# Optimization experiments

Measured on AMD Instinct MI355X. Metric: run time of the kernel, lower is better.

## Reference

```python
import jax, jax.numpy as jnp
import numpy as np

D_MODEL = 1024
N_HEADS = 16
N_KV_HEADS = 4
HEAD_DIM = 64


def setup_inputs() -> dict:
    key = jax.random.key(0)
    ks = jax.random.split(key, 5)
    B, T, P = 2, 512, 8
    scale = 1.0 / np.sqrt(D_MODEL)
    return {
        "hidden_states": jax.random.normal(ks[0], (B, T, P, D_MODEL), dtype=jnp.float32),
        # weights stored [in, out] so y = x @ W (same math as nn.Linear with W^T)
        "Wq": jax.random.normal(ks[1], (D_MODEL, N_HEADS * HEAD_DIM), dtype=jnp.float32) * scale,
        "Wk": jax.random.normal(ks[2], (D_MODEL, N_KV_HEADS * HEAD_DIM), dtype=jnp.float32) * scale,
        "Wv": jax.random.normal(ks[3], (D_MODEL, N_KV_HEADS * HEAD_DIM), dtype=jnp.float32) * scale,
        "Wo": jax.random.normal(ks[4], (N_HEADS * HEAD_DIM, D_MODEL), dtype=jnp.float32) * scale,
    }


def _rope_tables(T, d):
    half = d // 2
    inv_freq = 1.0 / (10000.0 ** (jnp.arange(half, dtype=jnp.float32) / half))
    pos = jnp.arange(T, dtype=jnp.float32)
    angles = pos[:, None] * inv_freq[None, :]  # (T, half)
    return jnp.cos(angles), jnp.sin(angles)


def _apply_rope(x, cos, sin):
    # x: (B, P, T, H, d); cos/sin: (T, d/2)
    half = x.shape[-1] // 2
    x1, x2 = x[..., :half], x[..., half:]
    c = cos[None, None, :, None, :]
    s = sin[None, None, :, None, :]
    return jnp.concatenate([x1 * c - x2 * s, x1 * s + x2 * c], axis=-1)


def reference(hidden_states, Wq, Wk, Wv, Wo):
    B, T, P, _ = hidden_states.shape
    x = jnp.transpose(hidden_states, (0, 2, 1, 3))  # (B, P, T, C)
    q = (x @ Wq).reshape(B, P, T, N_HEADS, HEAD_DIM)
    k = (x @ Wk).reshape(B, P, T, N_KV_HEADS, HEAD_DIM)
    v = (x @ Wv).reshape(B, P, T, N_KV_HEADS, HEAD_DIM)

    rep = N_HEADS // N_KV_HEADS
    k = jnp.repeat(k, rep, axis=3)  # (B,P,T,H,d) interleaved like torch repeat/view
    v = jnp.repeat(v, rep, axis=3)

    cos, sin = _rope_tables(T, HEAD_DIM)
    q = _apply_rope(q, cos, sin)
    k = _apply_rope(k, cos, sin)

    # (B,P,H,T,d)
    q = jnp.transpose(q, (0, 1, 3, 2, 4))
    k = jnp.transpose(k, (0, 1, 3, 2, 4))
    v = jnp.transpose(v, (0, 1, 3, 2, 4))

    attn = jnp.einsum("bphqd,bphkd->bphqk", q, k) / jnp.sqrt(
        jnp.asarray(HEAD_DIM, q.dtype))
    attn = jax.nn.softmax(attn, axis=-1)
    out = jnp.einsum("bphqk,bphkd->bphqd", attn, v)
    out = jnp.transpose(out, (0, 1, 3, 2, 4)).reshape(B, P, T, N_HEADS * HEAD_DIM)
    out = jnp.transpose(out, (0, 2, 1, 3))  # (B, T, P, H*d)
    return out @ Wo
```

## Files before the change

### kernel.cpp

```cpp
#include <hip/hip_runtime.h>
#include <hip/hip_bf16.h>
#include <stdint.h>


typedef __attribute__((ext_vector_type(8))) short bf16x8;
typedef __attribute__((ext_vector_type(4))) float f32x4;
typedef __attribute__((ext_vector_type(16))) float f32x16;
typedef __attribute__((ext_vector_type(4))) unsigned short us4;
typedef __attribute__((ext_vector_type(8))) unsigned short us8;

static __device__ __forceinline__ unsigned short f2bf(float f) {
  unsigned u = __float_as_uint(f);
  u += 0x7fffu + ((u >> 16) & 1u);
  return (unsigned short)(u >> 16);
}

static __device__ __forceinline__ us8 pack8(float4 a, float4 b) {
  union { __hip_bfloat162 h[4]; us8 v; } u;
  u.h[0] = __float22bfloat162_rn(make_float2(a.x, a.y));
  u.h[1] = __float22bfloat162_rn(make_float2(a.z, a.w));
  u.h[2] = __float22bfloat162_rn(make_float2(b.x, b.y));
  u.h[3] = __float22bfloat162_rn(make_float2(b.z, b.w));
  return u.v;
}

static __device__ __forceinline__ void ld_lds16(const void* g, void* l) {
  __builtin_amdgcn_global_load_lds(
      (const __attribute__((address_space(1))) void*)g,
      (__attribute__((address_space(3))) void*)l, 16, 0, 0);
}

static __device__ __forceinline__ f32x4 mfma16(bf16x8 a, bf16x8 b, f32x4 c) {
  return __builtin_amdgcn_mfma_f32_16x16x32_bf16(a, b, c, 0, 0, 0);
}
static __device__ __forceinline__ f32x16 mfma32(bf16x8 a, bf16x8 b, f32x16 c) {
  return __builtin_amdgcn_mfma_f32_32x32x16_bf16(a, b, c, 0, 0, 0);
}

__global__ __launch_bounds__(256) void conv_w(
    const float* __restrict__ Wq, const float* __restrict__ Wk,
    const float* __restrict__ Wv, const float* __restrict__ Wo,
    unsigned short* __restrict__ wqkv, unsigned short* __restrict__ wot) {
  __shared__ float tile[64][65];
  int tb = blockIdx.x, tid = threadIdx.x;
  const float* W; unsigned short* Wt; int N, tc0, tn0;
  if (tb < 256)      { W = Wq; Wt = wqkv;                       N = 1024; tc0 = (tb >> 4) * 64;          tn0 = (tb & 15) * 64; }
  else if (tb < 320) { W = Wk; Wt = wqkv + (size_t)1024 * 1024; N = 256;  tc0 = ((tb - 256) >> 2) * 64;  tn0 = ((tb - 256) & 3) * 64; }
  else if (tb < 384) { W = Wv; Wt = wqkv + (size_t)1280 * 1024; N = 256;  tc0 = ((tb - 320) >> 2) * 64;  tn0 = ((tb - 320) & 3) * 64; }
  else               { W = Wo; Wt = wot;                        N = 1024; tc0 = ((tb - 384) >> 4) * 64;  tn0 = ((tb - 384) & 15) * 64; }
  int tr = tid >> 4, tc = tid & 15;
#pragma unroll
  for (int i = 0; i < 4; ++i) {
    int c = tr + i * 16;
    float4 v = *(const float4*)(W + (size_t)(tc0 + c) * N + tn0 + tc * 4);
    tile[c][tc * 4 + 0] = v.x; tile[c][tc * 4 + 1] = v.y;
    tile[c][tc * 4 + 2] = v.z; tile[c][tc * 4 + 3] = v.w;
  }
  __syncthreads();
#pragma unroll
  for (int i = 0; i < 4; ++i) {
    int n = tr + i * 16;
    us4 o;
    o.x = f2bf(tile[tc * 4 + 0][n]); o.y = f2bf(tile[tc * 4 + 1][n]);
    o.z = f2bf(tile[tc * 4 + 2][n]); o.w = f2bf(tile[tc * 4 + 3][n]);
    *(us4*)(Wt + (size_t)(tn0 + n) * 1024 + tc0 + tc * 4) = o;
  }
}

template <int NT, int MODE>
__global__ __launch_bounds__(256, 3) void gemm_bt(
    const float* __restrict__ Af, const unsigned short* __restrict__ A,
    const unsigned short* __restrict__ Bt,
    unsigned short* __restrict__ qb, unsigned short* __restrict__ kb,
    unsigned short* __restrict__ vtb, float* __restrict__ out) {
  constexpr int K = 1024;
  __shared__ __align__(16) unsigned short Sm[128 * 128];
  unsigned short* As = Sm;
  unsigned short* Bs = Sm + 128 * 64;
  unsigned short* Cs = Sm;

  int tid = threadIdx.x;
  int lane = tid & 63, wid = tid >> 6;
  int quad = lane >> 4, lo = lane & 15;
  int tm = blockIdx.x & 63, tn = blockIdx.x >> 6;
  int wm = (wid >> 1) * 64, wn = (wid & 1) * 64;
  int srow = lane >> 3, schunk = lane & 7;

  f32x4 z = {0.f, 0.f, 0.f, 0.f};
  f32x4 acc[4][4];
  for (int i = 0; i < 4; ++i) for (int j = 0; j < 4; ++j) acc[i][j] = z;

  int cg = schunk ^ srow;
  int rowl = wid * 8 + srow;
  const unsigned short* pb = Bt + ((size_t)(tn * 128) + rowl) * K + cg * 8;
  char* dA = (char*)As + (wid * 8) * 128 + lane * 16;
  char* dB = (char*)Bs + (wid * 8) * 128 + lane * 16;

  const float* pax = nullptr;
  const unsigned short* pa = nullptr;
  if constexpr (MODE == 0) {
    int bp = tm >> 2, tt = tm & 3, b = bp >> 3, p = bp & 7;
    pax = Af + ((size_t)b * 4096 + (size_t)(tt * 128 + rowl) * 8 + p) * 1024 + cg * 8;
  } else {
    pa = A + ((size_t)(tm * 128) + rowl) * K + cg * 8;
  }

  float4 raf[8];
  us8 ra[4], rb[4];
#pragma unroll
  for (int i = 0; i < 4; ++i) {
    if constexpr (MODE == 0) {
      raf[2 * i]     = *(const float4*)(pax + (size_t)i * 32 * 8192);
      raf[2 * i + 1] = *(const float4*)(pax + (size_t)i * 32 * 8192 + 4);
    } else {
      ra[i] = *(const us8*)(pa + (size_t)i * 32 * K);
    }
    rb[i] = *(const us8*)(pb + (size_t)i * 32 * K);
  }

  for (int k0 = 0; k0 < K; k0 += 64) {
    __syncthreads();
#pragma unroll
    for (int i = 0; i < 4; ++i) {
      if constexpr (MODE == 0) {
        *(us8*)(dA + i * 32 * 128) = pack8(raf[2 * i], raf[2 * i + 1]);
      } else {
        *(us8*)(dA + i * 32 * 128) = ra[i];
      }
      *(us8*)(dB + i * 32 * 128) = rb[i];
    }
    __syncthreads();
    if (k0 + 64 < K) {
#pragma unroll
      for (int i = 0; i < 4; ++i) {
        if constexpr (MODE == 0) {
          raf[2 * i]     = *(const float4*)(pax + (size_t)i * 32 * 8192 + k0 + 64);
          raf[2 * i + 1] = *(const float4*)(pax + (size_t)i * 32 * 8192 + k0 + 68);
        } else {
          ra[i] = *(const us8*)(pa + (size_t)i * 32 * K + k0 + 64);
        }
        rb[i] = *(const us8*)(pb + (size_t)i * 32 * K + k0 + 64);
      }
    }
#pragma unroll
    for (int kk = 0; kk < 64; kk += 32) {
      bf16x8 af[4], bb[4];
#pragma unroll
      for (int mi = 0; mi < 4; ++mi) {
        int row = wm + mi * 16 + lo;
        int cgx = (quad + (kk >> 3)) ^ (row & 7);
        af[mi] = *(const bf16x8*)(As + (size_t)row * 64 + cgx * 8);
      }
#pragma unroll
      for (int ni = 0; ni < 4; ++ni) {
        int row = wn + ni * 16 + lo;
        int cgx = (quad + (kk >> 3)) ^ (row & 7);
        bb[ni] = *(const bf16x8*)(Bs + (size_t)row * 64 + cgx * 8);
      }
#pragma unroll
      for (int mi = 0; mi < 4; ++mi)
#pragma unroll
        for (int ni = 0; ni < 4; ++ni)
          acc[mi][ni] = mfma16(af[mi], bb[ni], acc[mi][ni]);
    }
  }

  __syncthreads();

  if (MODE == 0 && tn < 10) {
    float qscale = (tn < 8) ? 0.125f : 1.0f;
#pragma unroll
    for (int mi = 0; mi < 4; ++mi)
#pragma unroll
      for (int r = 0; r < 4; ++r) {
        int t = (tm * 128 + wm + mi * 16 + quad * 4 + r) & 511;
#pragma unroll
        for (int ni = 0; ni < 2; ++ni) {
          float inv = exp2f((float)(ni * 16 + lo) * -0.41524101186092029f);
          float ang = (float)t * inv;
          float s, c;
          __sincosf(ang, &s, &c);
          float x1 = acc[mi][ni][r], x2 = acc[mi][ni + 2][r];
          acc[mi][ni][r]     = (x1 * c - x2 * s) * qscale;
          acc[mi][ni + 2][r] = (x1 * s + x2 * c) * qscale;
        }
      }
#pragma unroll
    for (int mi = 0; mi < 4; ++mi)
#pragma unroll
      for (int ni = 0; ni < 4; ++ni)
#pragma unroll
        for (int r = 0; r < 4; ++r) {
          int row = wm + mi * 16 + quad * 4 + r;
          int col = wn + ni * 16 + lo;
          int cs = col ^ (((row >> 2) & 3) << 3);
          Cs[row * 128 + cs] = f2bf(acc[mi][ni][r]);
        }
    __syncthreads();
    int tc = tid & 15, ro = tid >> 4;
#pragma unroll
    for (int it = 0; it < 8; ++it) {
      int row = ro + 16 * it;
      int cs = (tc * 8) ^ (((row >> 2) & 3) << 3);
      us8 v = *(const us8*)(Cs + row * 128 + cs);
      size_t grow = (size_t)(tm * 128 + row);
      if (tn < 8) {
        *(us8*)(qb + grow * 1024 + tn * 128 + tc * 8) = v;
      } else {
        *(us8*)(kb + grow * 256 + (tn - 8) * 128 + tc * 8) = v;
      }
    }
  } else {
    for (int mi = 0; mi < 4; ++mi) {
      for (int ni = 0; ni < 4; ++ni) {
        int col = tn * 128 + wn + ni * 16 + lo;
        for (int r = 0; r < 4; ++r) {
          int grow = tm * 128 + wm + mi * 16 + quad * 4 + r;
          float val = acc[mi][ni][r];
          if (MODE == 0) {
            int cc = col - 1280;
            int hh = cc >> 6, dd = cc & 63;
            int bp = grow >> 9, t = grow & 511;
            vtb[(((size_t)(bp * 4 + hh)) * 64 + dd) * 512 + t] = f2bf(val);
          } else {
            int bp = grow >> 9, t = grow & 511;
            int b = bp >> 3, p = bp & 7;
            out[((((size_t)b * 512 + t) * 8 + p) << 10) + col] = val;
          }
        }
      }
    }
  }
}

__global__ __launch_bounds__(256, 4) void attn(
    const unsigned short* __restrict__ qb, const unsigned short* __restrict__ kb,
    const unsigned short* __restrict__ vtb, unsigned short* __restrict__ ao) {
  __shared__ __align__(16) unsigned short Qs[128 * 64];
  __shared__ __align__(16) unsigned short Ks[64 * 64];
  __shared__ __align__(16) unsigned short Vs[64 * 64];

  int tid = threadIdx.x;
  int lane = tid & 63, wid = tid >> 6;
  int lo32 = lane & 31, hl = lane >> 5;
  int qt = blockIdx.x & 3, bph = blockIdx.x >> 2;
  int head = bph & 15, bp = bph >> 4;
  int kvh = head >> 2;
  int t0 = qt * 128;
  int srow = lane >> 3, schunk = lane & 7;

  const unsigned short* qg = qb + ((size_t)(bp * 512 + t0)) * 1024 + head * 64;
  const unsigned short* kg = kb + ((size_t)bp * 512) * 256 + kvh * 64;
  const unsigned short* vg = vtb + ((size_t)(bp * 4 + kvh)) * 64 * 512;

  for (int i = 0; i < 4; ++i) {
    int row = wid * 8 + i * 32 + srow;
    int cgq = schunk ^ (row & 7);
    ld_lds16(qg + (size_t)row * 1024 + cgq * 8, (char*)Qs + (wid * 8 + i * 32) * 128);
  }

  int cg = schunk ^ srow;
  int row0 = wid * 8 + srow, row1 = row0 + 32;
  char* dK = (char*)Ks + (wid * 8) * 128 + lane * 16;
  char* dV = (char*)Vs + (wid * 8) * 128 + lane * 16;

  us8 rk[2], rv[2];
  rk[0] = *(const us8*)(kg + (size_t)row0 * 256 + cg * 8);
  rk[1] = *(const us8*)(kg + (size_t)row1 * 256 + cg * 8);
  rv[0] = *(const us8*)(vg + (size_t)row0 * 512 + cg * 8);
  rv[1] = *(const us8*)(vg + (size_t)row1 * 512 + cg * 8);

  f32x16 z16 = {0.f};
  f32x16 o0 = z16, o1 = z16;
  float psum = 0.f;
  int qrow = wid * 32 + lo32;

  for (int kt = 0; kt < 512; kt += 64) {
    __syncthreads();
    *(us8*)(dK) = rk[0];  *(us8*)(dK + 32 * 128) = rk[1];
    *(us8*)(dV) = rv[0];  *(us8*)(dV + 32 * 128) = rv[1];
    __syncthreads();
    if (kt + 64 < 512) {
      rk[0] = *(const us8*)(kg + (size_t)(kt + 64 + row0) * 256 + cg * 8);
      rk[1] = *(const us8*)(kg + (size_t)(kt + 64 + row1) * 256 + cg * 8);
      rv[0] = *(const us8*)(vg + (size_t)row0 * 512 + kt + 64 + cg * 8);
      rv[1] = *(const us8*)(vg + (size_t)row1 * 512 + kt + 64 + cg * 8);
    }

    f32x16 st0 = z16, st1 = z16;
#pragma unroll
    for (int kkc = 0; kkc < 4; ++kkc) {
      int ch = 2 * kkc + hl;
      bf16x8 qf = *(const bf16x8*)(Qs + (size_t)qrow * 64 + ((ch ^ (qrow & 7)) * 8));
      bf16x8 kf0 = *(const bf16x8*)(Ks + (size_t)lo32 * 64 + ((ch ^ (lo32 & 7)) * 8));
      bf16x8 kf1 = *(const bf16x8*)(Ks + (size_t)(32 + lo32) * 64 + ((ch ^ (lo32 & 7)) * 8));
      st0 = mfma32(kf0, qf, st0);
      st1 = mfma32(kf1, qf, st1);
    }

#pragma unroll
    for (int t = 0; t < 2; ++t) {
      const f32x16& stv = t ? st1 : st0;
      unsigned pk[8], xpk[8];
#pragma unroll
      for (int p = 0; p < 8; ++p) {
        float e0 = __expf(stv[2 * p]);
        float e1 = __expf(stv[2 * p + 1]);
        psum += e0 + e1;
        pk[p] = ((__float_as_uint(e0) + 0x8000u) >> 16) |
                ((__float_as_uint(e1) + 0x8000u) & 0xffff0000u);
      }
#pragma unroll
      for (int p = 0; p < 8; ++p) xpk[p] = (unsigned)__shfl_xor((int)pk[p], 32);
#pragma unroll
      for (int cc = 0; cc < 2; ++cc) {
        int o = cc * 4;
        union { unsigned u[4]; bf16x8 v; } af;
        if (hl == 0) {
          af.u[0] = pk[o];      af.u[1] = pk[o + 1];
          af.u[2] = xpk[o];     af.u[3] = xpk[o + 1];
        } else {
          af.u[0] = xpk[o + 2]; af.u[1] = xpk[o + 3];
          af.u[2] = pk[o + 2];  af.u[3] = pk[o + 3];
        }
        int vch = 2 * (t * 2 + cc) + hl;
        bf16x8 v0 = *(const bf16x8*)(Vs + (size_t)lo32 * 64 + ((vch ^ (lo32 & 7)) * 8));
        bf16x8 v1 = *(const bf16x8*)(Vs + (size_t)(32 + lo32) * 64 + ((vch ^ (lo32 & 7)) * 8));
        o0 = mfma32(af.v, v0, o0);
        o1 = mfma32(af.v, v1, o1);
      }
    }
  }

  psum += __shfl_xor(psum, 32);
  float inv = 1.f / psum;
#pragma unroll
  for (int r = 0; r < 16; ++r) {
    int q_r = (r & 3) + 8 * (r >> 2) + 4 * hl;
    float sc = __shfl(inv, q_r);
    size_t grow = (size_t)(bp * 512 + t0 + wid * 32 + q_r);
    ao[grow * 1024 + head * 64 + lo32]      = f2bf(o0[r] * sc);
    ao[grow * 1024 + head * 64 + 32 + lo32] = f2bf(o1[r] * sc);
  }
}

extern "C" void kernel_launch(void* const* d_in, const int* in_sizes, int n_in,
                              void* d_out, int out_size, void* d_ws, size_t ws_size,
                              hipStream_t stream) {
  const float* hs = (const float*)d_in[0];
  const float* Wq = (const float*)d_in[1];
  const float* Wk = (const float*)d_in[2];
  const float* Wv = (const float*)d_in[3];
  const float* Wo = (const float*)d_in[4];
  float* out = (float*)d_out;

  unsigned short* wqkv = (unsigned short*)d_ws;
  unsigned short* wot  = wqkv + (size_t)1536 * 1024;
  unsigned short* qbuf = wot + (size_t)1024 * 1024;
  unsigned short* kbuf = qbuf + (size_t)8192 * 1024;
  unsigned short* vtb  = kbuf + (size_t)8192 * 256;
  unsigned short* ao   = vtb + (size_t)8192 * 256;

  conv_w<<<640, 256, 0, stream>>>(Wq, Wk, Wv, Wo, wqkv, wot);
  gemm_bt<12, 0><<<768, 256, 0, stream>>>(hs, nullptr, wqkv, qbuf, kbuf, vtb, nullptr);
  attn<<<1024, 256, 0, stream>>>(qbuf, kbuf, vtb, ao);
  gemm_bt<8, 1><<<512, 256, 0, stream>>>(nullptr, ao, wot, nullptr, nullptr, nullptr, out);
}
```

Baseline: 183.9 us.

## Halve GEMM N-tile to 64 and move RoPE into LDS readback epilogue

```diff
diff --git a/kernel.cpp b/kernel.cpp
--- a/kernel.cpp
+++ b/kernel.cpp
@@ -13,6 +13,9 @@
   unsigned u = __float_as_uint(f);
   u += 0x7fffu + ((u >> 16) & 1u);
   return (unsigned short)(u >> 16);
+}
+static __device__ __forceinline__ float bf2f(unsigned short s) {
+  return __uint_as_float(((unsigned)s) << 16);
 }
 
 static __device__ __forceinline__ us8 pack8(float4 a, float4 b) {
@@ -68,13 +71,13 @@
 }
 
 template <int NT, int MODE>
-__global__ __launch_bounds__(256, 3) void gemm_bt(
+__global__ __launch_bounds__(256, 4) void gemm_bt(
     const float* __restrict__ Af, const unsigned short* __restrict__ A,
     const unsigned short* __restrict__ Bt,
     unsigned short* __restrict__ qb, unsigned short* __restrict__ kb,
     unsigned short* __restrict__ vtb, float* __restrict__ out) {
   constexpr int K = 1024;
-  __shared__ __align__(16) unsigned short Sm[128 * 128];
+  __shared__ __align__(16) unsigned short Sm[128 * 64 + 64 * 64];
   unsigned short* As = Sm;
   unsigned short* Bs = Sm + 128 * 64;
   unsigned short* Cs = Sm;
@@ -83,16 +86,16 @@
   int lane = tid & 63, wid = tid >> 6;
   int quad = lane >> 4, lo = lane & 15;
   int tm = blockIdx.x & 63, tn = blockIdx.x >> 6;
-  int wm = (wid >> 1) * 64, wn = (wid & 1) * 64;
+  int wm = (wid >> 1) * 64, wn = (wid & 1) * 32;
   int srow = lane >> 3, schunk = lane & 7;
 
   f32x4 z = {0.f, 0.f, 0.f, 0.f};
-  f32x4 acc[4][4];
-  for (int i = 0; i < 4; ++i) for (int j = 0; j < 4; ++j) acc[i][j] = z;
+  f32x4 acc[4][2];
+  for (int i = 0; i < 4; ++i) for (int j = 0; j < 2; ++j) acc[i][j] = z;
 
   int cg = schunk ^ srow;
   int rowl = wid * 8 + srow;
-  const unsigned short* pb = Bt + ((size_t)(tn * 128) + rowl) * K + cg * 8;
+  const unsigned short* pb = Bt + ((size_t)(tn * 64) + rowl) * K + cg * 8;
   char* dA = (char*)As + (wid * 8) * 128 + lane * 16;
   char* dB = (char*)Bs + (wid * 8) * 128 + lane * 16;
 
@@ -106,7 +109,7 @@
   }
 
   float4 raf[8];
-  us8 ra[4], rb[4];
+  us8 ra[4], rb[2];
 #pragma unroll
   for (int i = 0; i < 4; ++i) {
     if constexpr (MODE == 0) {
@@ -115,8 +118,10 @@
     } else {
       ra[i] = *(const us8*)(pa + (size_t)i * 32 * K);
     }
+  }
+#pragma unroll
+  for (int i = 0; i < 2; ++i)
     rb[i] = *(const us8*)(pb + (size_t)i * 32 * K);
-  }
 
   for (int k0 = 0; k0 < K; k0 += 64) {
     __syncthreads();
@@ -127,8 +132,9 @@
       } else {
         *(us8*)(dA + i * 32 * 128) = ra[i];
       }
-      *(us8*)(dB + i * 32 * 128) = rb[i];
-    }
+    }
+#pragma unroll
+    for (int i = 0; i < 2; ++i) *(us8*)(dB + i * 32 * 128) = rb[i];
     __syncthreads();
     if (k0 + 64 < K) {
 #pragma unroll
@@ -139,12 +145,14 @@
         } else {
           ra[i] = *(const us8*)(pa + (size_t)i * 32 * K + k0 + 64);
         }
+      }
+#pragma unroll
+      for (int i = 0; i < 2; ++i)
         rb[i] = *(const us8*)(pb + (size_t)i * 32 * K + k0 + 64);
-      }
     }
 #pragma unroll
     for (int kk = 0; kk < 64; kk += 32) {
-      bf16x8 af[4], bb[4];
+      bf16x8 af[4], bb[2];
 #pragma unroll
       for (int mi = 0; mi < 4; ++mi) {
         int row = wm + mi * 16 + lo;
@@ -152,7 +160,7 @@
         af[mi] = *(const bf16x8*)(As + (size_t)row * 64 + cgx * 8);
       }
 #pragma unroll
-      for (int ni = 0; ni < 4; ++ni) {
+      for (int ni = 0; ni < 2; ++ni) {
         int row = wn + ni * 16 + lo;
         int cgx = (quad + (kk >> 3)) ^ (row & 7);
         bb[ni] = *(const bf16x8*)(Bs + (size_t)row * 64 + cgx * 8);
@@ -160,60 +168,62 @@
 #pragma unroll
       for (int mi = 0; mi < 4; ++mi)
 #pragma unroll
-        for (int ni = 0; ni < 4; ++ni)
+        for (int ni = 0; ni < 2; ++ni)
           acc[mi][ni] = mfma16(af[mi], bb[ni], acc[mi][ni]);
     }
   }
 
   __syncthreads();
 
-  if (MODE == 0 && tn < 10) {
-    float qscale = (tn < 8) ? 0.125f : 1.0f;
+  if (MODE == 0 && tn < 20) {
 #pragma unroll
     for (int mi = 0; mi < 4; ++mi)
 #pragma unroll
-      for (int r = 0; r < 4; ++r) {
-        int t = (tm * 128 + wm + mi * 16 + quad * 4 + r) & 511;
-#pragma unroll
-        for (int ni = 0; ni < 2; ++ni) {
-          float inv = exp2f((float)(ni * 16 + lo) * -0.41524101186092029f);
-          float ang = (float)t * inv;
-          float s, c;
-          __sincosf(ang, &s, &c);
-          float x1 = acc[mi][ni][r], x2 = acc[mi][ni + 2][r];
-          acc[mi][ni][r]     = (x1 * c - x2 * s) * qscale;
-          acc[mi][ni + 2][r] = (x1 * s + x2 * c) * qscale;
-        }
-      }
-#pragma unroll
-    for (int mi = 0; mi < 4; ++mi)
-#pragma unroll
-      for (int ni = 0; ni < 4; ++ni)
+      for (int ni = 0; ni < 2; ++ni)
 #pragma unroll
         for (int r = 0; r < 4; ++r) {
           int row = wm + mi * 16 + quad * 4 + r;
           int col = wn + ni * 16 + lo;
           int cs = col ^ (((row >> 2) & 3) << 3);
-          Cs[row * 128 + cs] = f2bf(acc[mi][ni][r]);
+          Cs[row * 64 + cs] = f2bf(acc[mi][ni][r]);
         }
     __syncthreads();
-    int tc = tid & 15, ro = tid >> 4;
-#pragma unroll
-    for (int it = 0; it < 8; ++it) {
-      int row = ro + 16 * it;
-      int cs = (tc * 8) ^ (((row >> 2) & 3) << 3);
-      us8 v = *(const us8*)(Cs + row * 128 + cs);
+    float qscale = (tn < 16) ? 0.125f : 1.0f;
+    int tc = tid & 7, ro = tid >> 3;
+    float invf[8];
+#pragma unroll
+    for (int j = 0; j < 8; ++j)
+      invf[j] = exp2f((float)((tc * 8 + j) & 31) * -0.41524101186092029f);
+#pragma unroll
+    for (int it = 0; it < 4; ++it) {
+      int row = ro + 32 * it;
+      int s = ((row >> 2) & 3) << 3;
+      int pc = (tc * 8 + 32) & 63;
+      us8 a = *(const us8*)(Cs + row * 64 + ((tc * 8) ^ s));
+      us8 b = *(const us8*)(Cs + row * 64 + (pc ^ s));
+      int t = (tm * 128 + row) & 511;
+      us8 o;
+#pragma unroll
+      for (int j = 0; j < 8; ++j) {
+        float self = bf2f(((const unsigned short*)&a)[j]);
+        float oth  = bf2f(((const unsigned short*)&b)[j]);
+        float sn, cn;
+        __sincosf((float)t * invf[j], &sn, &cn);
+        int d = tc * 8 + j;
+        float v = (d < 32) ? (self * cn - oth * sn) : (oth * sn + self * cn);
+        ((unsigned short*)&o)[j] = f2bf(v * qscale);
+      }
       size_t grow = (size_t)(tm * 128 + row);
-      if (tn < 8) {
-        *(us8*)(qb + grow * 1024 + tn * 128 + tc * 8) = v;
+      if (tn < 16) {
+        *(us8*)(qb + grow * 1024 + tn * 64 + tc * 8) = o;
       } else {
-        *(us8*)(kb + grow * 256 + (tn - 8) * 128 + tc * 8) = v;
+        *(us8*)(kb + grow * 256 + (tn - 16) * 64 + tc * 8) = o;
       }
     }
   } else {
     for (int mi = 0; mi < 4; ++mi) {
-      for (int ni = 0; ni < 4; ++ni) {
-        int col = tn * 128 + wn + ni * 16 + lo;
+      for (int ni = 0; ni < 2; ++ni) {
+        int col = tn * 64 + wn + ni * 16 + lo;
         for (int r = 0; r < 4; ++r) {
           int grow = tm * 128 + wm + mi * 16 + quad * 4 + r;
           float val = acc[mi][ni][r];
@@ -362,7 +372,7 @@
   unsigned short* ao   = vtb + (size_t)8192 * 256;
 
   conv_w<<<640, 256, 0, stream>>>(Wq, Wk, Wv, Wo, wqkv, wot);
-  gemm_bt<12, 0><<<768, 256, 0, stream>>>(hs, nullptr, wqkv, qbuf, kbuf, vtb, nullptr);
+  gemm_bt<24, 0><<<1536, 256, 0, stream>>>(hs, nullptr, wqkv, qbuf, kbuf, vtb, nullptr);
   attn<<<1024, 256, 0, stream>>>(qbuf, kbuf, vtb, ao);
-  gemm_bt<8, 1><<<512, 256, 0, stream>>>(nullptr, ao, wot, nullptr, nullptr, nullptr, out);
-}
+  gemm_bt<16, 1><<<1024, 256, 0, stream>>>(nullptr, ao, wot, nullptr, nullptr, nullptr, out);
+}
```

Result: slower. 193.1 us (+5.0%).
